# Performance work log

Measured on AMD Instinct MI355X. Metric: run time of the kernel, lower is better.

Reference implementation:

```python
import jax, jax.numpy as jnp
import numpy as np

# Layer node counts: [n0, n1, n2, n3] for a 3-hop sampled subgraph
N_NODES = [524288, 65536, 8192, 1024]
DIMS = [100, 256, 256, 47]


def sage_conv(x_src, x_dst, src, dst, Wl, bl, Wr, n_dst):
    # PyG SAGEConv: lin_l(mean_agg(neighbors)) + lin_r(root)
    msg = x_src[src]                                        # [E, in]
    agg = jax.ops.segment_sum(msg, dst, num_segments=n_dst)  # [n_dst, in]
    cnt = jax.ops.segment_sum(jnp.ones((src.shape[0],), dtype=x_src.dtype), dst,
                              num_segments=n_dst)
    agg = agg / jnp.maximum(cnt, 1.0)[:, None]               # mean, 0-deg -> 0
    return agg @ Wl + bl + x_dst @ Wr


def setup_inputs() -> dict:
    key = jax.random.key(0)
    ks = jax.random.split(key, 20)
    inp = {"x": jax.random.normal(ks[0], (N_NODES[0], DIMS[0]), dtype=jnp.float32)}
    E = [655360, 81920, 10240]
    for i in range(3):
        inp[f"src{i}"] = jax.random.randint(ks[1 + 2 * i], (E[i],), 0, N_NODES[i])
        inp[f"dst{i}"] = jax.random.randint(ks[2 + 2 * i], (E[i],), 0, N_NODES[i + 1])
    for i in range(3):
        fin, fout = DIMS[i], DIMS[i + 1]
        inp[f"Wl{i}"] = jax.random.normal(ks[7 + 3 * i], (fin, fout), jnp.float32) * (1.0 / np.sqrt(fin))
        inp[f"bl{i}"] = jnp.zeros((fout,), jnp.float32)
        inp[f"Wr{i}"] = jax.random.normal(ks[8 + 3 * i], (fin, fout), jnp.float32) * (1.0 / np.sqrt(fin))
    return inp


def reference(x, src0, dst0, src1, dst1, src2, dst2,
              Wl0, bl0, Wr0, Wl1, bl1, Wr1, Wl2, bl2, Wr2):
    srcs = [src0, src1, src2]
    dsts = [dst0, dst1, dst2]
    Wls = [Wl0, Wl1, Wl2]
    bls = [bl0, bl1, bl2]
    Wrs = [Wr0, Wr1, Wr2]
    h = x
    for i in range(3):
        n_dst = N_NODES[i + 1]
        h_dst = h[:n_dst]
        h = sage_conv(h, h_dst, srcs[i], dsts[i], Wls[i], bls[i], Wrs[i], n_dst)
        if i != 2:
            h = jax.nn.relu(h)  # dropout is identity in eval mode
    return jax.nn.log_softmax(h, axis=-1)
```

## Files before the change

### kernel.cpp

```cpp
#include <hip/hip_runtime.h>
#include <math.h>

constexpr int NN1 = 65536, NN2 = 8192, NN3 = 1024;
constexpr int E0 = 655360, E1 = 81920, E2 = 10240;
constexpr int ETOT = E0 + E1 + E2;
constexpr int NTOT = NN1 + NN2 + NN3;

static inline int cdiv(int a, int b) { return (a + b - 1) / b; }

typedef __bf16 bf16x8_t __attribute__((ext_vector_type(8)));
typedef float f32x4_t __attribute__((ext_vector_type(4)));

__device__ __forceinline__ unsigned short f2bf(float f) {
    union { float f; unsigned int u; } v; v.f = f;
    unsigned int r = v.u + 0x7fffu + ((v.u >> 16) & 1u);
    return (unsigned short)(r >> 16);
}
__device__ __forceinline__ float bf2f(unsigned short h) {
    union { unsigned int u; float f; } v; v.u = ((unsigned int)h) << 16;
    return v.f;
}

constexpr int CB = (ETOT + 255) / 256;
__global__ void count_prep(const int* __restrict__ dst0, const int* __restrict__ dst1,
                           const int* __restrict__ dst2, int* __restrict__ cnt,
                           const float* __restrict__ Wl0, const float* __restrict__ Wr0,
                           unsigned short* __restrict__ Wt0a, unsigned short* __restrict__ Wt0b,
                           const float* __restrict__ Wl1, const float* __restrict__ Wr1,
                           unsigned short* __restrict__ Wt1a, unsigned short* __restrict__ Wt1b) {
    int b = blockIdx.x, t = threadIdx.x;
    if (b < CB) {
        int i = b * 256 + t;
        if (i < E0) atomicAdd(&cnt[dst0[i]], 1);
        else if (i < E0 + E1) atomicAdd(&cnt[NN1 + dst1[i - E0]], 1);
        else if (i < ETOT) atomicAdd(&cnt[NN1 + NN2 + dst2[i - E0 - E1]], 1);
        return;
    }
    b -= CB;
    if (b < 128) {
        int idx = b * 256 + t; int n = idx >> 7, k = idx & 127;
        Wt0a[idx] = f2bf(k < 100 ? Wl0[k * 256 + n] : 0.f);
    } else if (b < 256) {
        int idx = (b - 128) * 256 + t; int n = idx >> 7, k = idx & 127;
        Wt0b[idx] = f2bf(k < 100 ? Wr0[k * 256 + n] : 0.f);
    } else if (b < 512) {
        int idx = (b - 256) * 256 + t; int n = idx >> 8, k = idx & 255;
        Wt1a[idx] = f2bf(Wl1[k * 256 + n]);
    } else {
        int idx = (b - 512) * 256 + t; int n = idx >> 8, k = idx & 255;
        Wt1b[idx] = f2bf(Wr1[k * 256 + n]);
    }
}

__global__ __launch_bounds__(1024) void scan1(const int* __restrict__ cnt, int n,
                                              int* __restrict__ ofs, int* __restrict__ sums) {
    __shared__ int s[1024];
    int i = blockIdx.x * 1024 + threadIdx.x;
    int v = (i < n) ? cnt[i] : 0;
    s[threadIdx.x] = v;
    __syncthreads();
    for (int off = 1; off < 1024; off <<= 1) {
        int t = (threadIdx.x >= off) ? s[threadIdx.x - off] : 0;
        __syncthreads();
        s[threadIdx.x] += t;
        __syncthreads();
    }
    if (i < n) ofs[i] = s[threadIdx.x] - v;
    if (threadIdx.x == 1023) sums[blockIdx.x] = s[1023];
}

__global__ void scan3(const int* __restrict__ sums, int n,
                      int* __restrict__ ofs, int* __restrict__ cursor) {
    __shared__ int pref_s;
    int c = (blockIdx.x * 256) >> 10;
    if (threadIdx.x < 64) {
        int v = 0;
        for (int j = threadIdx.x; j < c; j += 64) v += sums[j];
        for (int o = 32; o; o >>= 1) v += __shfl_down(v, o);
        if (threadIdx.x == 0) pref_s = v;
    }
    __syncthreads();
    int i = blockIdx.x * 256 + threadIdx.x;
    if (i < n) {
        int v = ofs[i] + pref_s;
        ofs[i] = v;
        cursor[i] = v;
    }
    if (blockIdx.x == 0 && threadIdx.x == 0) ofs[n] = ETOT;
}

__global__ void scatter_all(const int* __restrict__ src0, const int* __restrict__ dst0,
                            const int* __restrict__ src1, const int* __restrict__ dst1,
                            const int* __restrict__ src2, const int* __restrict__ dst2,
                            int* __restrict__ cursor, int* __restrict__ perm) {
    int i = blockIdx.x * 256 + threadIdx.x;
    if (i < E0) {
        int p = atomicAdd(&cursor[dst0[i]], 1);
        perm[p] = src0[i];
    } else if (i < E0 + E1) {
        int j = i - E0;
        int p = atomicAdd(&cursor[NN1 + dst1[j]], 1);
        perm[p] = src1[j];
    } else if (i < ETOT) {
        int j = i - E0 - E1;
        int p = atomicAdd(&cursor[NN1 + NN2 + dst2[j]], 1);
        perm[p] = src2[j];
    }
}

__global__ __launch_bounds__(512) void fused_l0(const float* __restrict__ x,
                                                const int* __restrict__ perm,
                                                const int* __restrict__ ofs,
                                                const unsigned short* __restrict__ Wt0a,
                                                const unsigned short* __restrict__ Wt0b,
                                                const float* __restrict__ bias,
                                                unsigned short* __restrict__ h1) {
    __shared__ unsigned short As[128][136];
    int tid = threadIdx.x;
    int lane = tid & 63, wid = tid >> 6;
    int bm = blockIdx.x * 128;

    {
        int g = lane >> 5, l5 = lane & 31;
        bool act = l5 < 25;
        int node0 = bm + wid * 16;
        int myofs = (lane < 17) ? ofs[node0 + lane] : 0;

        int s0a = __shfl(myofs, 0);
        int s0b = __shfl(myofs, 1);
        int s1b = __shfl(myofs, 2);
        int dega = s0b - s0a, degb = s1b - s0b;
        int dca = min(dega, 64), dcb = min(degb, 64);
        int pea = (lane < dca) ? perm[s0a + lane] : 0;
        int peb = (lane < dcb) ? perm[s0b + lane] : 0;

        for (int r = 0; r < 16; r += 2) {
            int s0a_n = 0, s0b_n = 0, dega_n = 0, degb_n = 0, dca_n = 0, dcb_n = 0;
            int pea_n = 0, peb_n = 0;
            if (r + 2 < 16) {
                s0a_n = __shfl(myofs, r + 2);
                s0b_n = __shfl(myofs, r + 3);
                int s1b_n = __shfl(myofs, r + 4);
                dega_n = s0b_n - s0a_n; degb_n = s1b_n - s0b_n;
                dca_n = min(dega_n, 64); dcb_n = min(degb_n, 64);
                pea_n = (lane < dca_n) ? perm[s0a_n + lane] : 0;
                peb_n = (lane < dcb_n) ? perm[s0b_n + lane] : 0;
            }
            f32x4_t A0 = {0.f, 0.f, 0.f, 0.f}, A1 = A0, A2 = A0, A3 = A0;
            f32x4_t B0 = A0, B1 = A0, B2 = A0, B3 = A0;
            int mx = max(dca, dcb);
            for (int b = 0; b < mx; b += 8) {
                int e0 = b + g, e1 = b + 2 + g, e2 = b + 4 + g, e3 = b + 6 + g;
                int pa0 = __shfl(pea, e0), pa1 = __shfl(pea, e1);
                int pa2 = __shfl(pea, e2), pa3 = __shfl(pea, e3);
                int pb0 = __shfl(peb, e0), pb1 = __shfl(peb, e1);
                int pb2 = __shfl(peb, e2), pb3 = __shfl(peb, e3);
                f32x4_t z = {0.f, 0.f, 0.f, 0.f};
                f32x4_t va0 = z, va1 = z, va2 = z, va3 = z;
                f32x4_t vb0 = z, vb1 = z, vb2 = z, vb3 = z;
                if (act && e0 < dca) va0 = *reinterpret_cast<const f32x4_t*>(x + (size_t)pa0 * 100 + l5 * 4);
                if (act && e1 < dca) va1 = *reinterpret_cast<const f32x4_t*>(x + (size_t)pa1 * 100 + l5 * 4);
                if (act && e2 < dca) va2 = *reinterpret_cast<const f32x4_t*>(x + (size_t)pa2 * 100 + l5 * 4);
                if (act && e3 < dca) va3 = *reinterpret_cast<const f32x4_t*>(x + (size_t)pa3 * 100 + l5 * 4);
                if (act && e0 < dcb) vb0 = *reinterpret_cast<const f32x4_t*>(x + (size_t)pb0 * 100 + l5 * 4);
                if (act && e1 < dcb) vb1 = *reinterpret_cast<const f32x4_t*>(x + (size_t)pb1 * 100 + l5 * 4);
                if (act && e2 < dcb) vb2 = *reinterpret_cast<const f32x4_t*>(x + (size_t)pb2 * 100 + l5 * 4);
                if (act && e3 < dcb) vb3 = *reinterpret_cast<const f32x4_t*>(x + (size_t)pb3 * 100 + l5 * 4);
                A0 += va0; A1 += va1; A2 += va2; A3 += va3;
                B0 += vb0; B1 += vb1; B2 += vb2; B3 += vb3;
            }
            for (int e = s0a + 64; e < s0a + dega; e += 2) {
                int idx = e + g;
                if (act && idx < s0a + dega)
                    A0 += *reinterpret_cast<const f32x4_t*>(x + (size_t)perm[idx] * 100 + l5 * 4);
            }
            for (int e = s0b + 64; e < s0b + degb; e += 2) {
                int idx = e + g;
                if (act && idx < s0b + degb)
                    B0 += *reinterpret_cast<const f32x4_t*>(x + (size_t)perm[idx] * 100 + l5 * 4);
            }
            f32x4_t a = (A0 + A1) + (A2 + A3);
            f32x4_t bb = (B0 + B1) + (B2 + B3);
#pragma unroll
            for (int c = 0; c < 4; c++) {
                a[c] += __shfl_xor(a[c], 32);
                bb[c] += __shfl_xor(bb[c], 32);
            }
            float inva = 1.0f / fmaxf((float)dega, 1.0f);
            float invb = 1.0f / fmaxf((float)degb, 1.0f);
            int rowa = wid * 16 + r, rowb = rowa + 1;
            if (lane < 25) {
                ushort4 oa, ob;
                oa.x = f2bf(a[0] * inva); oa.y = f2bf(a[1] * inva);
                oa.z = f2bf(a[2] * inva); oa.w = f2bf(a[3] * inva);
                ob.x = f2bf(bb[0] * invb); ob.y = f2bf(bb[1] * invb);
                ob.z = f2bf(bb[2] * invb); ob.w = f2bf(bb[3] * invb);
                *reinterpret_cast<ushort4*>(&As[rowa][lane * 4]) = oa;
                *reinterpret_cast<ushort4*>(&As[rowb][lane * 4]) = ob;
            } else if (lane < 32) {
                ushort4 z4 = make_ushort4(0, 0, 0, 0);
                *reinterpret_cast<ushort4*>(&As[rowa][100 + (lane - 25) * 4]) = z4;
                *reinterpret_cast<ushort4*>(&As[rowb][100 + (lane - 25) * 4]) = z4;
            }
            s0a = s0a_n; s0b = s0b_n; dega = dega_n; degb = degb_n;
            dca = dca_n; dcb = dcb_n; pea = pea_n; peb = peb_n;
        }
    }

    f32x4_t acc[4][4];
#pragma unroll
    for (int i = 0; i < 4; i++)
#pragma unroll
        for (int j = 0; j < 4; j++)
#pragma unroll
            for (int r = 0; r < 4; r++) acc[i][j][r] = 0.f;

    int r0 = lane & 15, kg = lane >> 4;
    int wm = (wid >> 2) * 64, wn = (wid & 3) * 64;

    for (int pass = 0; pass < 2; ++pass) {
        const unsigned short* W = pass ? Wt0b : Wt0a;
        if (pass) {
            __syncthreads();
            int rown = tid >> 2, q = tid & 3;
            for (int c4 = q; c4 < 25; c4 += 4) {
                f32x4_t v = *reinterpret_cast<const f32x4_t*>(x + (size_t)(bm + rown) * 100 + c4 * 4);
                ushort4 o;
                o.x = f2bf(v[0]); o.y = f2bf(v[1]); o.z = f2bf(v[2]); o.w = f2bf(v[3]);
                *reinterpret_cast<ushort4*>(&As[rown][c4 * 4]) = o;
            }
            if (q == 3) {
#pragma unroll
                for (int c4 = 25; c4 < 32; ++c4)
                    *reinterpret_cast<ushort4*>(&As[rown][c4 * 4]) = make_ushort4(0, 0, 0, 0);
            }
        }
        __syncthreads();
#pragma unroll
        for (int ks = 0; ks < 4; ++ks) {
            bf16x8_t af[4], bfv[4];
#pragma unroll
            for (int ni = 0; ni < 4; ni++)
                bfv[ni] = *reinterpret_cast<const bf16x8_t*>(&W[(size_t)(wn + ni * 16 + r0) * 128 + ks * 32 + kg * 8]);
#pragma unroll
            for (int mi = 0; mi < 4; mi++)
                af[mi] = *reinterpret_cast<const bf16x8_t*>(&As[wm + mi * 16 + r0][ks * 32 + kg * 8]);
#pragma unroll
            for (int mi = 0; mi < 4; mi++)
#pragma unroll
                for (int ni = 0; ni < 4; ni++)
                    acc[mi][ni] = __builtin_amdgcn_mfma_f32_16x16x32_bf16(af[mi], bfv[ni], acc[mi][ni], 0, 0, 0);
        }
    }

    int cc = lane & 15, rr = (lane >> 4) * 4;
#pragma unroll
    for (int mi = 0; mi < 4; mi++) {
#pragma unroll
        for (int ni = 0; ni < 4; ni++) {
            int col = wn + ni * 16 + cc;
            float b = bias[col];
#pragma unroll
            for (int j = 0; j < 4; j++) {
                int row = bm + wm + mi * 16 + rr + j;
                float v = fmaxf(acc[mi][ni][j] + b, 0.f);
                h1[(size_t)row * 256 + col] = f2bf(v);
            }
        }
    }
}

__global__ __launch_bounds__(512) void fused_l1(const unsigned short* __restrict__ h1,
                                                const int* __restrict__ perm,
                                                const int* __restrict__ ofs,
                                                const unsigned short* __restrict__ Wt1a,
                                                const unsigned short* __restrict__ Wt1b,
                                                const float* __restrict__ bias,
                                                float* __restrict__ h2) {
    __shared__ unsigned short As[32][264];
    int tid = threadIdx.x;
    int lane = tid & 63, wid = tid >> 6;
    int bm = blockIdx.x * 32;

    {
        int node0 = bm + wid * 4;
        int myofs = (lane < 5) ? ofs[node0 + lane] : 0;
        int s0a = __shfl(myofs, 0);
        int s0b = __shfl(myofs, 1);
        int s1b = __shfl(myofs, 2);
        int dega = s0b - s0a, degb = s1b - s0b;
        int dca = min(dega, 64), dcb = min(degb, 64);
        int pea = (lane < dca) ? perm[s0a + lane] : 0;
        int peb = (lane < dcb) ? perm[s0b + lane] : 0;

        for (int r = 0; r < 4; r += 2) {
            int s0a_n = 0, s0b_n = 0, dega_n = 0, degb_n = 0, dca_n = 0, dcb_n = 0;
            int pea_n = 0, peb_n = 0;
            if (r + 2 < 4) {
                s0a_n = __shfl(myofs, 2);
                s0b_n = __shfl(myofs, 3);
                int s1b_n = __shfl(myofs, 4);
                dega_n = s0b_n - s0a_n; degb_n = s1b_n - s0b_n;
                dca_n = min(dega_n, 64); dcb_n = min(degb_n, 64);
                pea_n = (lane < dca_n) ? perm[s0a_n + lane] : 0;
                peb_n = (lane < dcb_n) ? perm[s0b_n + lane] : 0;
            }
            float aca[4][4] = {}, acb[4][4] = {};
            int mx = max(dca, dcb);
            for (int b = 0; b < mx; b += 4) {
#pragma unroll
                for (int u = 0; u < 4; u++) {
                    int pau = __shfl(pea, b + u);
                    int pbu = __shfl(peb, b + u);
                    ushort4 va = make_ushort4(0, 0, 0, 0), vb = va;
                    if (b + u < dca) va = *reinterpret_cast<const ushort4*>(h1 + (size_t)pau * 256 + lane * 4);
                    if (b + u < dcb) vb = *reinterpret_cast<const ushort4*>(h1 + (size_t)pbu * 256 + lane * 4);
                    aca[u][0] += bf2f(va.x); aca[u][1] += bf2f(va.y);
                    aca[u][2] += bf2f(va.z); aca[u][3] += bf2f(va.w);
                    acb[u][0] += bf2f(vb.x); acb[u][1] += bf2f(vb.y);
                    acb[u][2] += bf2f(vb.z); acb[u][3] += bf2f(vb.w);
                }
            }
            for (int e = s0a + 64; e < s0a + dega; e++) {
                ushort4 v = *reinterpret_cast<const ushort4*>(h1 + (size_t)perm[e] * 256 + lane * 4);
                aca[0][0] += bf2f(v.x); aca[0][1] += bf2f(v.y);
                aca[0][2] += bf2f(v.z); aca[0][3] += bf2f(v.w);
            }
            for (int e = s0b + 64; e < s0b + degb; e++) {
                ushort4 v = *reinterpret_cast<const ushort4*>(h1 + (size_t)perm[e] * 256 + lane * 4);
                acb[0][0] += bf2f(v.x); acb[0][1] += bf2f(v.y);
                acb[0][2] += bf2f(v.z); acb[0][3] += bf2f(v.w);
            }
            float inva = 1.0f / fmaxf((float)dega, 1.0f);
            float invb = 1.0f / fmaxf((float)degb, 1.0f);
            ushort4 oa, ob;
            oa.x = f2bf((aca[0][0] + aca[1][0] + aca[2][0] + aca[3][0]) * inva);
            oa.y = f2bf((aca[0][1] + aca[1][1] + aca[2][1] + aca[3][1]) * inva);
            oa.z = f2bf((aca[0][2] + aca[1][2] + aca[2][2] + aca[3][2]) * inva);
            oa.w = f2bf((aca[0][3] + aca[1][3] + aca[2][3] + aca[3][3]) * inva);
            ob.x = f2bf((acb[0][0] + acb[1][0] + acb[2][0] + acb[3][0]) * invb);
            ob.y = f2bf((acb[0][1] + acb[1][1] + acb[2][1] + acb[3][1]) * invb);
            ob.z = f2bf((acb[0][2] + acb[1][2] + acb[2][2] + acb[3][2]) * invb);
            ob.w = f2bf((acb[0][3] + acb[1][3] + acb[2][3] + acb[3][3]) * invb);
            *reinterpret_cast<ushort4*>(&As[wid * 4 + r][lane * 4]) = oa;
            *reinterpret_cast<ushort4*>(&As[wid * 4 + r + 1][lane * 4]) = ob;
            s0a = s0a_n; s0b = s0b_n; dega = dega_n; degb = degb_n;
            dca = dca_n; dcb = dcb_n; pea = pea_n; peb = peb_n;
        }
    }

    f32x4_t acc[2][2];
#pragma unroll
    for (int i = 0; i < 2; i++)
#pragma unroll
        for (int j = 0; j < 2; j++)
#pragma unroll
            for (int r = 0; r < 4; r++) acc[i][j][r] = 0.f;

    int r0 = lane & 15, kg = lane >> 4;
    int wn = wid * 32;

    for (int pass = 0; pass < 2; ++pass) {
        const unsigned short* W = pass ? Wt1b : Wt1a;
        if (pass) {
            __syncthreads();
            for (int c = tid; c < 1024; c += 512) {
                int row = c >> 5, k8 = (c & 31) << 3;
                *reinterpret_cast<int4*>(&As[row][k8]) =
                    *reinterpret_cast<const int4*>(&h1[(size_t)(bm + row) * 256 + k8]);
            }
        }
        __syncthreads();
#pragma unroll
        for (int ks = 0; ks < 8; ++ks) {
            bf16x8_t af[2], bfv[2];
#pragma unroll
            for (int ni = 0; ni < 2; ni++)
                bfv[ni] = *reinterpret_cast<const bf16x8_t*>(&W[(size_t)(wn + ni * 16 + r0) * 256 + ks * 32 + kg * 8]);
#pragma unroll
            for (int mi = 0; mi < 2; mi++)
                af[mi] = *reinterpret_cast<const bf16x8_t*>(&As[mi * 16 + r0][ks * 32 + kg * 8]);
#pragma unroll
            for (int mi = 0; mi < 2; mi++)
#pragma unroll
                for (int ni = 0; ni < 2; ni++)
                    acc[mi][ni] = __builtin_amdgcn_mfma_f32_16x16x32_bf16(af[mi], bfv[ni], acc[mi][ni], 0, 0, 0);
        }
    }

    int cc = lane & 15, rr = (lane >> 4) * 4;
#pragma unroll
    for (int mi = 0; mi < 2; mi++) {
#pragma unroll
        for (int ni = 0; ni < 2; ni++) {
            int col = wn + ni * 16 + cc;
            float b = bias[col];
#pragma unroll
            for (int j = 0; j < 4; j++) {
                int row = bm + mi * 16 + rr + j;
                h2[(size_t)row * 256 + col] = fmaxf(acc[mi][ni][j] + b, 0.f);
            }
        }
    }
}

__global__ void agg_vec4_256(const float* __restrict__ x, const int* __restrict__ perm,
                             const int* __restrict__ ofs, float* __restrict__ agg, int nrows) {
    int wave = (blockIdx.x * blockDim.x + threadIdx.x) >> 6;
    int lane = threadIdx.x & 63;
    if (wave >= nrows) return;
    int s0 = ofs[wave], s1 = ofs[wave + 1];
    float4 acc = make_float4(0.f, 0.f, 0.f, 0.f);
    for (int e = s0; e < s1; e++) {
        const float4* xr = (const float4*)(x + (size_t)perm[e] * 256);
        float4 v = xr[lane];
        acc.x += v.x; acc.y += v.y; acc.z += v.z; acc.w += v.w;
    }
    float inv = 1.0f / fmaxf((float)(s1 - s0), 1.0f);
    acc.x *= inv; acc.y *= inv; acc.z *= inv; acc.w *= inv;
    ((float4*)(agg + (size_t)wave * 256))[lane] = acc;
}

__global__ __launch_bounds__(256) void gemm2_fused(const float* __restrict__ A1, const float* __restrict__ W1, int K1,
                                                   const float* __restrict__ A2, const float* __restrict__ W2, int K2,
                                                   const float* __restrict__ bias, float* __restrict__ out,
                                                   int M, int N) {
    __shared__ float As[16][65];
    __shared__ float Bs[16][64];
    int tid = threadIdx.x;
    int tx = tid & 15, ty = tid >> 4;
    int bm = blockIdx.y * 64;
    float acc[4][4] = {};
    for (int pass = 0; pass < 2; ++pass) {
        const float* A = pass ? A2 : A1;
        const float* W = pass ? W2 : W1;
        int K = pass ? K2 : K1;
        for (int k0 = 0; k0 < K; k0 += 16) {
#pragma unroll
            for (int i = 0; i < 4; i++) {
                int L = i * 256 + tid;
                int m = L >> 4, k = L & 15;
                int gm = bm + m, gk = k0 + k;
                float v = 0.f;
                if (gm < M && gk < K) v = A[(size_t)gm * K + gk];
                As[k][m] = v;
            }
#pragma unroll
            for (int i = 0; i < 4; i++) {
                int L = i * 256 + tid;
                int n = L & 63, k = L >> 6;
                int gk = k0 + k;
                float v = 0.f;
                if (gk < K && n < N) v = W[(size_t)gk * N + n];
                Bs[k][n] = v;
            }
            __syncthreads();
#pragma unroll
            for (int k = 0; k < 16; k++) {
                float a[4], b[4];
#pragma unroll
                for (int i = 0; i < 4; i++) a[i] = As[k][ty * 4 + i];
#pragma unroll
                for (int j = 0; j < 4; j++) b[j] = Bs[k][tx * 4 + j];
#pragma unroll
                for (int i = 0; i < 4; i++)
#pragma unroll
                    for (int j = 0; j < 4; j++) acc[i][j] += a[i] * b[j];
            }
            __syncthreads();
        }
    }
#pragma unroll
    for (int i = 0; i < 4; i++) {
        int gm = bm + ty * 4 + i;
        float vals[4];
        float vmax = -1e30f;
#pragma unroll
        for (int j = 0; j < 4; j++) {
            int gn = tx * 4 + j;
            vals[j] = (gn < N) ? acc[i][j] + bias[gn] : -1e30f;
            vmax = fmaxf(vmax, vals[j]);
        }
#pragma unroll
        for (int o = 1; o < 16; o <<= 1) vmax = fmaxf(vmax, __shfl_xor(vmax, o));
        float se = 0.f;
#pragma unroll
        for (int j = 0; j < 4; j++) {
            int gn = tx * 4 + j;
            if (gn < N) se += expf(vals[j] - vmax);
        }
#pragma unroll
        for (int o = 1; o < 16; o <<= 1) se += __shfl_xor(se, o);
        float ls = logf(se);
#pragma unroll
        for (int j = 0; j < 4; j++) {
            int gn = tx * 4 + j;
            if (gn < N && gm < M) out[(size_t)gm * N + gn] = vals[j] - vmax - ls;
        }
    }
}

extern "C" void kernel_launch(void* const* d_in, const int* in_sizes, int n_in,
                              void* d_out, int out_size, void* d_ws, size_t ws_size,
                              hipStream_t stream) {
    const float* x   = (const float*)d_in[0];
    const int* src0  = (const int*)d_in[1];
    const int* dst0  = (const int*)d_in[2];
    const int* src1  = (const int*)d_in[3];
    const int* dst1  = (const int*)d_in[4];
    const int* src2  = (const int*)d_in[5];
    const int* dst2  = (const int*)d_in[6];
    const float* Wl0 = (const float*)d_in[7];
    const float* bl0 = (const float*)d_in[8];
    const float* Wr0 = (const float*)d_in[9];
    const float* Wl1 = (const float*)d_in[10];
    const float* bl1 = (const float*)d_in[11];
    const float* Wr1 = (const float*)d_in[12];
    const float* Wl2 = (const float*)d_in[13];
    const float* bl2 = (const float*)d_in[14];
    const float* Wr2 = (const float*)d_in[15];
    float* out = (float*)d_out;

    char* p = (char*)d_ws;
    auto alloc = [&](size_t bytes) { char* r = p; p += (bytes + 255) & ~(size_t)255; return r; };
    unsigned short* h1   = (unsigned short*)alloc((size_t)NN1 * 256 * 2);
    float* h2    = (float*)alloc((size_t)NN2 * 256 * 4);
    float* agg2  = (float*)alloc((size_t)NN3 * 256 * 4);
    unsigned short* Wt0a = (unsigned short*)alloc(256 * 128 * 2);
    unsigned short* Wt0b = (unsigned short*)alloc(256 * 128 * 2);
    unsigned short* Wt1a = (unsigned short*)alloc(256 * 256 * 2);
    unsigned short* Wt1b = (unsigned short*)alloc(256 * 256 * 2);
    int* cnt    = (int*)alloc((size_t)NTOT * 4);
    int* ofs    = (int*)alloc((size_t)(NTOT + 1) * 4);
    int* cursor = (int*)alloc((size_t)(NTOT + 1) * 4);
    int* sums   = (int*)alloc(128 * 4);
    int* perm   = (int*)alloc((size_t)ETOT * 4);

    hipMemsetAsync(cnt, 0, (size_t)NTOT * 4, stream);
    count_prep<<<CB + 768, 256, 0, stream>>>(dst0, dst1, dst2, cnt,
                                             Wl0, Wr0, Wt0a, Wt0b, Wl1, Wr1, Wt1a, Wt1b);
    int nb = cdiv(NTOT, 1024);
    scan1<<<nb, 1024, 0, stream>>>(cnt, NTOT, ofs, sums);
    scan3<<<cdiv(NTOT, 256), 256, 0, stream>>>(sums, NTOT, ofs, cursor);
    scatter_all<<<cdiv(ETOT, 256), 256, 0, stream>>>(src0, dst0, src1, dst1, src2, dst2, cursor, perm);

    fused_l0<<<NN1 / 128, 512, 0, stream>>>(x, perm, ofs, Wt0a, Wt0b, bl0, h1);

    fused_l1<<<NN2 / 32, 512, 0, stream>>>(h1, perm, ofs + NN1, Wt1a, Wt1b, bl1, h2);

    agg_vec4_256<<<cdiv(NN3 * 64, 256), 256, 0, stream>>>(h2, perm, ofs + NN1 + NN2, agg2, NN3);
    {
        dim3 grid(1, NN3 / 64);
        gemm2_fused<<<grid, 256, 0, stream>>>(agg2, Wl2, 256, h2, Wr2, 256, bl2, out, NN3, 47);
    }
}
```

Measured before the change: 290.7 us.

## Halve layer-0 block tile to 64 rows and stage weights through LDS

```diff
diff --git a/kernel.cpp b/kernel.cpp
--- a/kernel.cpp
+++ b/kernel.cpp
@@ -115,16 +115,17 @@
                                                 const unsigned short* __restrict__ Wt0b,
                                                 const float* __restrict__ bias,
                                                 unsigned short* __restrict__ h1) {
-    __shared__ unsigned short As[128][136];
+    __shared__ unsigned short As[64][136];
+    __shared__ unsigned short Bs[256][40];
     int tid = threadIdx.x;
     int lane = tid & 63, wid = tid >> 6;
-    int bm = blockIdx.x * 128;
+    int bm = blockIdx.x * 64;
 
     {
         int g = lane >> 5, l5 = lane & 31;
         bool act = l5 < 25;
-        int node0 = bm + wid * 16;
-        int myofs = (lane < 17) ? ofs[node0 + lane] : 0;
+        int node0 = bm + wid * 8;
+        int myofs = (lane < 9) ? ofs[node0 + lane] : 0;
 
         int s0a = __shfl(myofs, 0);
         int s0b = __shfl(myofs, 1);
@@ -134,10 +135,10 @@
         int pea = (lane < dca) ? perm[s0a + lane] : 0;
         int peb = (lane < dcb) ? perm[s0b + lane] : 0;
 
-        for (int r = 0; r < 16; r += 2) {
+        for (int r = 0; r < 8; r += 2) {
             int s0a_n = 0, s0b_n = 0, dega_n = 0, degb_n = 0, dca_n = 0, dcb_n = 0;
             int pea_n = 0, peb_n = 0;
-            if (r + 2 < 16) {
+            if (r + 2 < 8) {
                 s0a_n = __shfl(myofs, r + 2);
                 s0b_n = __shfl(myofs, r + 3);
                 int s1b_n = __shfl(myofs, r + 4);
@@ -188,7 +189,7 @@
             }
             float inva = 1.0f / fmaxf((float)dega, 1.0f);
             float invb = 1.0f / fmaxf((float)degb, 1.0f);
-            int rowa = wid * 16 + r, rowb = rowa + 1;
+            int rowa = wid * 8 + r, rowb = rowa + 1;
             if (lane < 25) {
                 ushort4 oa, ob;
                 oa.x = f2bf(a[0] * inva); oa.y = f2bf(a[1] * inva);
@@ -207,48 +208,53 @@
         }
     }
 
-    f32x4_t acc[4][4];
+    f32x4_t acc[4][2];
 #pragma unroll
     for (int i = 0; i < 4; i++)
 #pragma unroll
-        for (int j = 0; j < 4; j++)
+        for (int j = 0; j < 2; j++)
 #pragma unroll
             for (int r = 0; r < 4; r++) acc[i][j][r] = 0.f;
 
     int r0 = lane & 15, kg = lane >> 4;
-    int wm = (wid >> 2) * 64, wn = (wid & 3) * 64;
+    int wn = wid * 32;
 
     for (int pass = 0; pass < 2; ++pass) {
         const unsigned short* W = pass ? Wt0b : Wt0a;
         if (pass) {
             __syncthreads();
-            int rown = tid >> 2, q = tid & 3;
-            for (int c4 = q; c4 < 25; c4 += 4) {
-                f32x4_t v = *reinterpret_cast<const f32x4_t*>(x + (size_t)(bm + rown) * 100 + c4 * 4);
-                ushort4 o;
-                o.x = f2bf(v[0]); o.y = f2bf(v[1]); o.z = f2bf(v[2]); o.w = f2bf(v[3]);
-                *reinterpret_cast<ushort4*>(&As[rown][c4 * 4]) = o;
-            }
-            if (q == 3) {
-#pragma unroll
-                for (int c4 = 25; c4 < 32; ++c4)
-                    *reinterpret_cast<ushort4*>(&As[rown][c4 * 4]) = make_ushort4(0, 0, 0, 0);
-            }
-        }
-        __syncthreads();
+            for (int c = tid; c < 2048; c += 512) {
+                int row = c >> 5, c4 = c & 31;
+                if (c4 < 25) {
+                    f32x4_t v = *reinterpret_cast<const f32x4_t*>(x + (size_t)(bm + row) * 100 + c4 * 4);
+                    ushort4 o;
+                    o.x = f2bf(v[0]); o.y = f2bf(v[1]); o.z = f2bf(v[2]); o.w = f2bf(v[3]);
+                    *reinterpret_cast<ushort4*>(&As[row][c4 * 4]) = o;
+                } else {
+                    *reinterpret_cast<ushort4*>(&As[row][c4 * 4]) = make_ushort4(0, 0, 0, 0);
+                }
+            }
+        }
 #pragma unroll
         for (int ks = 0; ks < 4; ++ks) {
-            bf16x8_t af[4], bfv[4];
-#pragma unroll
-            for (int ni = 0; ni < 4; ni++)
-                bfv[ni] = *reinterpret_cast<const bf16x8_t*>(&W[(size_t)(wn + ni * 16 + r0) * 128 + ks * 32 + kg * 8]);
+            __syncthreads();
+            for (int c = tid; c < 1024; c += 512) {
+                int n = c >> 2, k8 = (c & 3) << 3;
+                *reinterpret_cast<int4*>(&Bs[n][k8]) =
+                    *reinterpret_cast<const int4*>(&W[(size_t)n * 128 + ks * 32 + k8]);
+            }
+            __syncthreads();
+            bf16x8_t af[4], bfv[2];
+#pragma unroll
+            for (int ni = 0; ni < 2; ni++)
+                bfv[ni] = *reinterpret_cast<const bf16x8_t*>(&Bs[wn + ni * 16 + r0][kg * 8]);
 #pragma unroll
             for (int mi = 0; mi < 4; mi++)
-                af[mi] = *reinterpret_cast<const bf16x8_t*>(&As[wm + mi * 16 + r0][ks * 32 + kg * 8]);
+                af[mi] = *reinterpret_cast<const bf16x8_t*>(&As[mi * 16 + r0][ks * 32 + kg * 8]);
 #pragma unroll
             for (int mi = 0; mi < 4; mi++)
 #pragma unroll
-                for (int ni = 0; ni < 4; ni++)
+                for (int ni = 0; ni < 2; ni++)
                     acc[mi][ni] = __builtin_amdgcn_mfma_f32_16x16x32_bf16(af[mi], bfv[ni], acc[mi][ni], 0, 0, 0);
         }
     }
@@ -257,12 +263,12 @@
 #pragma unroll
     for (int mi = 0; mi < 4; mi++) {
 #pragma unroll
-        for (int ni = 0; ni < 4; ni++) {
+        for (int ni = 0; ni < 2; ni++) {
             int col = wn + ni * 16 + cc;
             float b = bias[col];
 #pragma unroll
             for (int j = 0; j < 4; j++) {
-                int row = bm + wm + mi * 16 + rr + j;
+                int row = bm + mi * 16 + rr + j;
                 float v = fmaxf(acc[mi][ni][j] + b, 0.f);
                 h1[(size_t)row * 256 + col] = f2bf(v);
             }
@@ -544,7 +550,7 @@
     scan3<<<cdiv(NTOT, 256), 256, 0, stream>>>(sums, NTOT, ofs, cursor);
     scatter_all<<<cdiv(ETOT, 256), 256, 0, stream>>>(src0, dst0, src1, dst1, src2, dst2, cursor, perm);
 
-    fused_l0<<<NN1 / 128, 512, 0, stream>>>(x, perm, ofs, Wt0a, Wt0b, bl0, h1);
+    fused_l0<<<NN1 / 64, 512, 0, stream>>>(x, perm, ofs, Wt0a, Wt0b, bl0, h1);
 
     fused_l1<<<NN2 / 32, 512, 0, stream>>>(h1, perm, ofs + NN1, Wt1a, Wt1b, bl1, h2);
 
```

Result: faster. 283.9 us (-2.3%).
